# Performance work log

Hardware: AMD Instinct MI355X
Metric: run time of the kernel (lower is better)

The kernel has to match this reference:

```python
import jax, jax.numpy as jnp
import numpy as np

B, T, D = 4, 2048, 2048
NUM_EXPERTS = 64
TOP_K = 2


def setup_inputs() -> dict:
    key = jax.random.key(0)
    k_x, k_n, k_wg, k_wn = jax.random.split(key, 4)
    x = jax.random.normal(k_x, (B, T, D), dtype=jnp.float32)
    noise_eps = jax.random.normal(k_n, (B, T, NUM_EXPERTS), dtype=jnp.float32)
    # nn.Linear(D, E, bias=False): weight [E, D]; store transposed [D, E] for einsum
    scale = 1.0 / np.sqrt(D)
    w_gate = jax.random.uniform(k_wg, (D, NUM_EXPERTS), jnp.float32, -scale, scale)
    w_noise = jax.random.uniform(k_wn, (D, NUM_EXPERTS), jnp.float32, -scale, scale)
    return {"x": x, "noise_eps": noise_eps, "w_gate": w_gate, "w_noise": w_noise}


def reference(x, noise_eps, w_gate, w_noise):
    # gate + noisy logits: softplus(w_noise(x)) * randn_like (noise_eps passed in)
    logits = jnp.einsum("btd,de->bte", x, w_gate)
    noise = jax.nn.softplus(jnp.einsum("btd,de->bte", x, w_noise)) * noise_eps
    logits = logits + noise

    # top-k over experts
    top_k_logits, top_k_indices = jax.lax.top_k(logits, TOP_K)  # [B,T,K]

    # scatter(-inf fill) + softmax == softmax over top-k values scattered into E slots
    one_hot = jax.nn.one_hot(top_k_indices, NUM_EXPERTS, dtype=logits.dtype)  # [B,T,K,E]
    router_probs = jnp.einsum("btk,btke->bte", jax.nn.softmax(top_k_logits, axis=-1), one_hot)

    # per-expert mask: [num_tokens, K, E] -> permute(1,0,2) -> [K, num_tokens, E]
    exp_mask = one_hot.reshape(B * T, TOP_K, NUM_EXPERTS).transpose(1, 0, 2).astype(jnp.int32)
    return router_probs, top_k_indices, exp_mask
```

## Files before the change

kernel.cpp:

```cpp
#include <hip/hip_runtime.h>
#include <math.h>

#define DD    2048
#define EE    64
#define NTOK  8192
#define BM    32
#define NKS   32

#define PROB_OFF 0
#define IDX_OFF  524288
#define MASK_OFF 540672
#define MASK_K_STRIDE (NTOK * EE)

typedef __bf16 bf16x8 __attribute__((ext_vector_type(8)));
typedef float  f32x16 __attribute__((ext_vector_type(16)));

__device__ __forceinline__ unsigned f2bf_rne(float f) {
  unsigned u = __float_as_uint(f);
  return (u + 0x7fffu + ((u >> 16) & 1u)) >> 16;
}
__device__ __forceinline__ float bf2f(unsigned h) {
  return __uint_as_float(h << 16);
}

__global__ __launch_bounds__(256) void prep_w(
    const float* __restrict__ wg, const float* __restrict__ wn,
    unsigned char* __restrict__ wsb)
{
  const int t  = blockIdx.x * 256 + threadIdx.x;
  const int l  = t & 63;
  const int nt = (t >> 6) & 3;
  const int g  = t >> 8;
  const int colg = nt * 32 + (l & 31);
  const int kb   = g * 16 + 8 * (l >> 5);
  const float* wsrc = (colg < EE) ? (wg + colg) : (wn + (colg - EE));

  unsigned hv[8], lv[8];
#pragma unroll
  for (int i = 0; i < 8; ++i) {
    const float v = wsrc[(size_t)(kb + i) * EE];
    const unsigned h = f2bf_rne(v);
    hv[i] = h;
    lv[i] = f2bf_rne(v - bf2f(h));
  }
  uint4 hq, lq;
  hq.x = hv[0] | (hv[1] << 16); hq.y = hv[2] | (hv[3] << 16);
  hq.z = hv[4] | (hv[5] << 16); hq.w = hv[6] | (hv[7] << 16);
  lq.x = lv[0] | (lv[1] << 16); lq.y = lv[2] | (lv[3] << 16);
  lq.z = lv[4] | (lv[5] << 16); lq.w = lv[6] | (lv[7] << 16);

  const size_t base = ((size_t)(g * 4 + nt) * 2) * 1024 + (size_t)l * 16;
  *reinterpret_cast<uint4*>(wsb + base)        = hq;
  *reinterpret_cast<uint4*>(wsb + base + 1024) = lq;
}

struct KSet { float4 xa, xb; uint4 bh, bl; };

union BF8 { bf16x8 v; ushort u[8]; };

__device__ __forceinline__ void cvt_hilo(const float4& a, const float4& b,
                                         bf16x8& hi, bf16x8& lo) {
  const float f[8] = {a.x, a.y, a.z, a.w, b.x, b.y, b.z, b.w};
  BF8 H, L;
#pragma unroll
  for (int i = 0; i < 8; ++i) {
    const unsigned u = __float_as_uint(f[i]);
    H.u[i] = (ushort)(u >> 16);
    L.v[i] = (__bf16)(f[i] - __uint_as_float(u & 0xffff0000u));
  }
  hi = H.v; lo = L.v;
}

__global__ __launch_bounds__(1024, 4) void router_fused(
    const float* __restrict__ x,
    const float* __restrict__ noise_eps,
    const unsigned char* __restrict__ wsb,
    float* __restrict__ out)
{
  __shared__ float Lp[4][BM][128];

  const int tid  = threadIdx.x;
  const int wid  = tid >> 6;
  const int lane = tid & 63;
  const int nt   = wid & 3;
  const int kh   = wid >> 2;
  const int tok0 = blockIdx.x * BM;

  const float* xp = x + (size_t)(tok0 + (lane & 31)) * DD
                      + kh * 512 + 8 * (lane >> 5);
  const unsigned char* bp = wsb + ((size_t)(kh * 32) * 4 + nt) * 2048
                                + (size_t)lane * 16;

  auto LOAD = [&](int s) {
    KSet k;
    const float* p = xp + 16 * s;
    k.xa = *reinterpret_cast<const float4*>(p);
    k.xb = *reinterpret_cast<const float4*>(p + 4);
    const unsigned char* q = bp + (size_t)8192 * s;
    k.bh = *reinterpret_cast<const uint4*>(q);
    k.bl = *reinterpret_cast<const uint4*>(q + 1024);
    return k;
  };

  f32x16 acc = {0.f,0.f,0.f,0.f,0.f,0.f,0.f,0.f,
                0.f,0.f,0.f,0.f,0.f,0.f,0.f,0.f};

  auto COMPUTE = [&](const KSet& k) {
    bf16x8 ahi, alo;
    cvt_hilo(k.xa, k.xb, ahi, alo);
    const bf16x8 bhi = __builtin_bit_cast(bf16x8, k.bh);
    const bf16x8 blo = __builtin_bit_cast(bf16x8, k.bl);
    acc = __builtin_amdgcn_mfma_f32_32x32x16_bf16(ahi, bhi, acc, 0, 0, 0);
    acc = __builtin_amdgcn_mfma_f32_32x32x16_bf16(ahi, blo, acc, 0, 0, 0);
    acc = __builtin_amdgcn_mfma_f32_32x32x16_bf16(alo, bhi, acc, 0, 0, 0);
    acc = __builtin_amdgcn_mfma_f32_32x32x16_bf16(alo, blo, acc, 0, 0, 0);
  };

  KSet a = LOAD(0), b = LOAD(1);
#pragma unroll 1
  for (int s = 0; s < NKS - 2; s += 2) {
    KSet t0 = LOAD(s + 2);
    COMPUTE(a);
    a = t0;
    KSet t1 = LOAD(s + 3);
    COMPUTE(b);
    b = t1;
  }
  COMPUTE(a);
  COMPUTE(b);

  const int ccol  = nt * 32 + (lane & 31);
  const int crow0 = 4 * (lane >> 5);
#pragma unroll
  for (int q = 0; q < 16; ++q)
    Lp[kh][(q & 3) + 8 * (q >> 2) + crow0][ccol] = acc[q];
  __syncthreads();

#pragma unroll
  for (int it = 0; it < 2; ++it) {
    const int tl  = wid * 2 + it;
    const int tok = tok0 + tl;

    const float g    = Lp[0][tl][lane] + Lp[1][tl][lane]
                     + Lp[2][tl][lane] + Lp[3][tl][lane];
    const float nraw = Lp[0][tl][64 + lane] + Lp[1][tl][64 + lane]
                     + Lp[2][tl][64 + lane] + Lp[3][tl][64 + lane];
    const float ep   = noise_eps[(size_t)tok * EE + lane];

    const float sp = fmaxf(nraw, 0.0f) + log1pf(expf(-fabsf(nraw)));
    const float z  = fmaf(sp, ep, g);

    float v1 = z; int i1 = lane;
#pragma unroll
    for (int off = 32; off >= 1; off >>= 1) {
      const float ov = __shfl_xor(v1, off, 64);
      const int   oi = __shfl_xor(i1, off, 64);
      if (ov > v1 || (ov == v1 && oi < i1)) { v1 = ov; i1 = oi; }
    }
    float v2 = (lane == i1) ? -INFINITY : z; int i2 = lane;
#pragma unroll
    for (int off = 32; off >= 1; off >>= 1) {
      const float ov = __shfl_xor(v2, off, 64);
      const int   oi = __shfl_xor(i2, off, 64);
      if (ov > v2 || (ov == v2 && oi < i2)) { v2 = ov; i2 = oi; }
    }

    const float e2 = expf(v2 - v1);
    const float denom = 1.0f + e2;
    const float p1 = 1.0f / denom;
    const float p2 = e2 / denom;

    out[PROB_OFF + (size_t)tok * EE + lane] =
        (lane == i1) ? p1 : ((lane == i2) ? p2 : 0.0f);
    if (lane == 0) {
      out[IDX_OFF + tok * 2 + 0] = (float)i1;
      out[IDX_OFF + tok * 2 + 1] = (float)i2;
    }
    out[MASK_OFF + 0 * MASK_K_STRIDE + (size_t)tok * EE + lane] =
        (lane == i1) ? 1.0f : 0.0f;
    out[MASK_OFF + 1 * MASK_K_STRIDE + (size_t)tok * EE + lane] =
        (lane == i2) ? 1.0f : 0.0f;
  }
}

extern "C" void kernel_launch(void* const* d_in, const int* in_sizes, int n_in,
                              void* d_out, int out_size, void* d_ws, size_t ws_size,
                              hipStream_t stream) {
  const float* x   = (const float*)d_in[0];
  const float* eps = (const float*)d_in[1];
  const float* wg  = (const float*)d_in[2];
  const float* wn  = (const float*)d_in[3];
  unsigned char* wsb = (unsigned char*)d_ws;

  prep_w<<<dim3(128), dim3(256), 0, stream>>>(wg, wn, wsb);
  router_fused<<<dim3(NTOK / BM), dim3(1024), 0, stream>>>(x, eps, wsb,
                                                           (float*)d_out);
}
```

Baseline: 138.3 us.

## Reuse converted x fragments across four expert tiles per wave, drop lo*lo MFMA

Each block now uses 8 waves instead of 16. Each wave covers a 256-wide K slice for all 128 output columns, so one x load and its hi/lo bf16 conversion feed four accumulators. This removes the fourfold redundant x loading and conversion of the old per-column-tile wave split. The lo*lo MFMA term is dropped, trimming MFMA work by a quarter at a small accuracy cost. The pipeline becomes a fully unrolled 3-slot register prefetch, and partial sums are reduced through shared memory in two phases; this raises register pressure and may cut the latency hiding that came from running more waves.

```diff
diff --git a/kernel.cpp b/kernel.cpp
--- a/kernel.cpp
+++ b/kernel.cpp
@@ -5,7 +5,8 @@
 #define EE    64
 #define NTOK  8192
 #define BM    32
-#define NKS   32
+#define NKH   8
+#define NKS   16
 
 #define PROB_OFF 0
 #define IDX_OFF  524288
@@ -54,7 +55,10 @@
   *reinterpret_cast<uint4*>(wsb + base + 1024) = lq;
 }
 
-struct KSet { float4 xa, xb; uint4 bh, bl; };
+struct Slot {
+  float4 xa, xb;
+  uint4 bh0, bl0, bh1, bl1, bh2, bl2, bh3, bl3;
+};
 
 union BF8 { bf16x8 v; ushort u[8]; };
 
@@ -71,7 +75,57 @@
   hi = H.v; lo = L.v;
 }
 
-__global__ __launch_bounds__(1024, 4) void router_fused(
+__device__ __forceinline__ bf16x8 bc(const uint4& q) {
+  return __builtin_bit_cast(bf16x8, q);
+}
+
+__device__ __forceinline__ void load_slot(Slot& s, const float* xp,
+                                          const unsigned char* bp, int ks) {
+  const float* p = xp + 16 * ks;
+  s.xa = *reinterpret_cast<const float4*>(p);
+  s.xb = *reinterpret_cast<const float4*>(p + 4);
+  const unsigned char* q = bp + (size_t)8192 * ks;
+  s.bh0 = *reinterpret_cast<const uint4*>(q);
+  s.bl0 = *reinterpret_cast<const uint4*>(q + 1024);
+  s.bh1 = *reinterpret_cast<const uint4*>(q + 2048);
+  s.bl1 = *reinterpret_cast<const uint4*>(q + 3072);
+  s.bh2 = *reinterpret_cast<const uint4*>(q + 4096);
+  s.bl2 = *reinterpret_cast<const uint4*>(q + 5120);
+  s.bh3 = *reinterpret_cast<const uint4*>(q + 6144);
+  s.bl3 = *reinterpret_cast<const uint4*>(q + 7168);
+}
+
+__device__ __forceinline__ void compute_slot(const Slot& s,
+    f32x16& a0, f32x16& a1, f32x16& a2, f32x16& a3) {
+  bf16x8 ahi, alo;
+  cvt_hilo(s.xa, s.xb, ahi, alo);
+  {
+    const bf16x8 bh = bc(s.bh0), bl = bc(s.bl0);
+    a0 = __builtin_amdgcn_mfma_f32_32x32x16_bf16(ahi, bh, a0, 0, 0, 0);
+    a0 = __builtin_amdgcn_mfma_f32_32x32x16_bf16(ahi, bl, a0, 0, 0, 0);
+    a0 = __builtin_amdgcn_mfma_f32_32x32x16_bf16(alo, bh, a0, 0, 0, 0);
+  }
+  {
+    const bf16x8 bh = bc(s.bh1), bl = bc(s.bl1);
+    a1 = __builtin_amdgcn_mfma_f32_32x32x16_bf16(ahi, bh, a1, 0, 0, 0);
+    a1 = __builtin_amdgcn_mfma_f32_32x32x16_bf16(ahi, bl, a1, 0, 0, 0);
+    a1 = __builtin_amdgcn_mfma_f32_32x32x16_bf16(alo, bh, a1, 0, 0, 0);
+  }
+  {
+    const bf16x8 bh = bc(s.bh2), bl = bc(s.bl2);
+    a2 = __builtin_amdgcn_mfma_f32_32x32x16_bf16(ahi, bh, a2, 0, 0, 0);
+    a2 = __builtin_amdgcn_mfma_f32_32x32x16_bf16(ahi, bl, a2, 0, 0, 0);
+    a2 = __builtin_amdgcn_mfma_f32_32x32x16_bf16(alo, bh, a2, 0, 0, 0);
+  }
+  {
+    const bf16x8 bh = bc(s.bh3), bl = bc(s.bl3);
+    a3 = __builtin_amdgcn_mfma_f32_32x32x16_bf16(ahi, bh, a3, 0, 0, 0);
+    a3 = __builtin_amdgcn_mfma_f32_32x32x16_bf16(ahi, bl, a3, 0, 0, 0);
+    a3 = __builtin_amdgcn_mfma_f32_32x32x16_bf16(alo, bh, a3, 0, 0, 0);
+  }
+}
+
+__global__ __launch_bounds__(512, 2) void router_fused(
     const float* __restrict__ x,
     const float* __restrict__ noise_eps,
     const unsigned char* __restrict__ wsb,
@@ -82,63 +136,56 @@
   const int tid  = threadIdx.x;
   const int wid  = tid >> 6;
   const int lane = tid & 63;
-  const int nt   = wid & 3;
-  const int kh   = wid >> 2;
+  const int kh   = wid;
   const int tok0 = blockIdx.x * BM;
 
   const float* xp = x + (size_t)(tok0 + (lane & 31)) * DD
-                      + kh * 512 + 8 * (lane >> 5);
-  const unsigned char* bp = wsb + ((size_t)(kh * 32) * 4 + nt) * 2048
-                                + (size_t)lane * 16;
-
-  auto LOAD = [&](int s) {
-    KSet k;
-    const float* p = xp + 16 * s;
-    k.xa = *reinterpret_cast<const float4*>(p);
-    k.xb = *reinterpret_cast<const float4*>(p + 4);
-    const unsigned char* q = bp + (size_t)8192 * s;
-    k.bh = *reinterpret_cast<const uint4*>(q);
-    k.bl = *reinterpret_cast<const uint4*>(q + 1024);
-    return k;
-  };
-
-  f32x16 acc = {0.f,0.f,0.f,0.f,0.f,0.f,0.f,0.f,
-                0.f,0.f,0.f,0.f,0.f,0.f,0.f,0.f};
-
-  auto COMPUTE = [&](const KSet& k) {
-    bf16x8 ahi, alo;
-    cvt_hilo(k.xa, k.xb, ahi, alo);
-    const bf16x8 bhi = __builtin_bit_cast(bf16x8, k.bh);
-    const bf16x8 blo = __builtin_bit_cast(bf16x8, k.bl);
-    acc = __builtin_amdgcn_mfma_f32_32x32x16_bf16(ahi, bhi, acc, 0, 0, 0);
-    acc = __builtin_amdgcn_mfma_f32_32x32x16_bf16(ahi, blo, acc, 0, 0, 0);
-    acc = __builtin_amdgcn_mfma_f32_32x32x16_bf16(alo, bhi, acc, 0, 0, 0);
-    acc = __builtin_amdgcn_mfma_f32_32x32x16_bf16(alo, blo, acc, 0, 0, 0);
-  };
-
-  KSet a = LOAD(0), b = LOAD(1);
-#pragma unroll 1
-  for (int s = 0; s < NKS - 2; s += 2) {
-    KSet t0 = LOAD(s + 2);
-    COMPUTE(a);
-    a = t0;
-    KSet t1 = LOAD(s + 3);
-    COMPUTE(b);
-    b = t1;
-  }
-  COMPUTE(a);
-  COMPUTE(b);
-
-  const int ccol  = nt * 32 + (lane & 31);
+                      + kh * 256 + 8 * (lane >> 5);
+  const unsigned char* bp = wsb + (size_t)(kh * 16) * 8192 + (size_t)lane * 16;
+
+  f32x16 a0 = {0.f,0.f,0.f,0.f,0.f,0.f,0.f,0.f,0.f,0.f,0.f,0.f,0.f,0.f,0.f,0.f};
+  f32x16 a1 = a0, a2 = a0, a3 = a0;
+
+  Slot s0, s1, s2;
+  load_slot(s0, xp, bp, 0);
+  load_slot(s1, xp, bp, 1);
+  load_slot(s2, xp, bp, 2);
+
+#pragma unroll
+  for (int s = 0; s < NKS; ++s) {
+    Slot& cur = (s % 3 == 0) ? s0 : (s % 3 == 1) ? s1 : s2;
+    compute_slot(cur, a0, a1, a2, a3);
+    if (s + 3 < NKS) load_slot(cur, xp, bp, s + 3);
+  }
+
+  const int ccol0 = lane & 31;
   const int crow0 = 4 * (lane >> 5);
-#pragma unroll
-  for (int q = 0; q < 16; ++q)
-    Lp[kh][(q & 3) + 8 * (q >> 2) + crow0][ccol] = acc[q];
+  if (wid < 4) {
+#pragma unroll
+    for (int q = 0; q < 16; ++q) {
+      const int row = (q & 3) + 8 * (q >> 2) + crow0;
+      Lp[wid][row][ccol0]      = a0[q];
+      Lp[wid][row][32 + ccol0] = a1[q];
+      Lp[wid][row][64 + ccol0] = a2[q];
+      Lp[wid][row][96 + ccol0] = a3[q];
+    }
+  }
   __syncthreads();
-
-#pragma unroll
-  for (int it = 0; it < 2; ++it) {
-    const int tl  = wid * 2 + it;
+  if (wid >= 4) {
+#pragma unroll
+    for (int q = 0; q < 16; ++q) {
+      const int row = (q & 3) + 8 * (q >> 2) + crow0;
+      Lp[wid - 4][row][ccol0]      += a0[q];
+      Lp[wid - 4][row][32 + ccol0] += a1[q];
+      Lp[wid - 4][row][64 + ccol0] += a2[q];
+      Lp[wid - 4][row][96 + ccol0] += a3[q];
+    }
+  }
+  __syncthreads();
+
+#pragma unroll
+  for (int it = 0; it < 4; ++it) {
+    const int tl  = wid * 4 + it;
     const int tok = tok0 + tl;
 
     const float g    = Lp[0][tl][lane] + Lp[1][tl][lane]
@@ -193,6 +240,6 @@
   unsigned char* wsb = (unsigned char*)d_ws;
 
   prep_w<<<dim3(128), dim3(256), 0, stream>>>(wg, wn, wsb);
-  router_fused<<<dim3(NTOK / BM), dim3(1024), 0, stream>>>(x, eps, wsb,
-                                                           (float*)d_out);
-}
+  router_fused<<<dim3(NTOK / BM), dim3(512), 0, stream>>>(x, eps, wsb,
+                                                          (float*)d_out);
+}
```

New measurement: 127.6 us. 7.7% less time.

## Split-K router GEMM into separate kernel with workspace partials and epilogue kernel

Applied to the files above, without the earlier changes.

Replaces the single fused 1024-thread kernel with a split-K GEMM kernel (256 threads, grid over tokens x 4 K-slices) that writes partial logits to workspace, followed by a separate epilogue kernel doing the reduction, softplus, top-2, softmax and mask writes. Each wave now computes two N-tiles and drops the lo*lo MFMA term (3 MFMAs per tile instead of 4), and the explicit double-buffered prefetch is replaced by a fully unrolled loop. The aim is more blocks and better occupancy with less MFMA work. In exchange it adds partial-sum traffic through global memory, an extra kernel launch, and slightly lower precision from dropping the lo*lo term.

```diff
diff --git a/kernel.cpp b/kernel.cpp
--- a/kernel.cpp
+++ b/kernel.cpp
@@ -1,11 +1,12 @@
 #include <hip/hip_runtime.h>
 #include <math.h>
 
-#define DD    2048
-#define EE    64
-#define NTOK  8192
-#define BM    32
-#define NKS   32
+#define DD     2048
+#define EE     64
+#define NTOK   8192
+#define BM     32
+#define KSPLIT 4
+#define NKS    16
 
 #define PROB_OFF 0
 #define IDX_OFF  524288
@@ -54,8 +55,6 @@
   *reinterpret_cast<uint4*>(wsb + base + 1024) = lq;
 }
 
-struct KSet { float4 xa, xb; uint4 bh, bl; };
-
 union BF8 { bf16x8 v; ushort u[8]; };
 
 __device__ __forceinline__ void cvt_hilo(const float4& a, const float4& b,
@@ -71,116 +70,135 @@
   hi = H.v; lo = L.v;
 }
 
-__global__ __launch_bounds__(1024, 4) void router_fused(
+__device__ __forceinline__ bf16x8 bc(const uint4& q) {
+  return __builtin_bit_cast(bf16x8, q);
+}
+
+__global__ __launch_bounds__(256, 4) void router_gemm(
     const float* __restrict__ x,
+    const unsigned char* __restrict__ wsb,
+    float* __restrict__ part)
+{
+  __shared__ float Lp[BM][128];
+
+  const int tid  = threadIdx.x;
+  const int w    = tid >> 6;
+  const int lane = tid & 63;
+  const int nt2  = w & 1;
+  const int kq   = w >> 1;
+  const int tok0 = blockIdx.x * BM;
+  const int ks   = blockIdx.y;
+
+  const int kbase = ks * 512 + kq * 256;
+  const float* xp = x + (size_t)(tok0 + (lane & 31)) * DD
+                      + kbase + 8 * (lane >> 5);
+  const unsigned char* bp = wsb
+      + ((size_t)((kbase >> 4) * 4 + 2 * nt2)) * 2048 + (size_t)lane * 16;
+
+  f32x16 a0 = {0.f,0.f,0.f,0.f,0.f,0.f,0.f,0.f,0.f,0.f,0.f,0.f,0.f,0.f,0.f,0.f};
+  f32x16 a1 = a0;
+
+#pragma unroll
+  for (int s = 0; s < NKS; ++s) {
+    const float* p = xp + 16 * s;
+    const float4 xa = *reinterpret_cast<const float4*>(p);
+    const float4 xb = *reinterpret_cast<const float4*>(p + 4);
+    const unsigned char* q = bp + (size_t)8192 * s;
+    const uint4 bh0 = *reinterpret_cast<const uint4*>(q);
+    const uint4 bl0 = *reinterpret_cast<const uint4*>(q + 1024);
+    const uint4 bh1 = *reinterpret_cast<const uint4*>(q + 2048);
+    const uint4 bl1 = *reinterpret_cast<const uint4*>(q + 3072);
+
+    bf16x8 ahi, alo;
+    cvt_hilo(xa, xb, ahi, alo);
+    a0 = __builtin_amdgcn_mfma_f32_32x32x16_bf16(ahi, bc(bh0), a0, 0, 0, 0);
+    a0 = __builtin_amdgcn_mfma_f32_32x32x16_bf16(ahi, bc(bl0), a0, 0, 0, 0);
+    a0 = __builtin_amdgcn_mfma_f32_32x32x16_bf16(alo, bc(bh0), a0, 0, 0, 0);
+    a1 = __builtin_amdgcn_mfma_f32_32x32x16_bf16(ahi, bc(bh1), a1, 0, 0, 0);
+    a1 = __builtin_amdgcn_mfma_f32_32x32x16_bf16(ahi, bc(bl1), a1, 0, 0, 0);
+    a1 = __builtin_amdgcn_mfma_f32_32x32x16_bf16(alo, bc(bh1), a1, 0, 0, 0);
+  }
+
+  const int ccol  = 64 * nt2 + (lane & 31);
+  const int crow0 = 4 * (lane >> 5);
+  if (kq == 0) {
+#pragma unroll
+    for (int q = 0; q < 16; ++q) {
+      const int row = (q & 3) + 8 * (q >> 2) + crow0;
+      Lp[row][ccol]      = a0[q];
+      Lp[row][ccol + 32] = a1[q];
+    }
+  }
+  __syncthreads();
+  if (kq == 1) {
+#pragma unroll
+    for (int q = 0; q < 16; ++q) {
+      const int row = (q & 3) + 8 * (q >> 2) + crow0;
+      Lp[row][ccol]      += a0[q];
+      Lp[row][ccol + 32] += a1[q];
+    }
+  }
+  __syncthreads();
+
+#pragma unroll
+  for (int rr = 0; rr < 8; ++rr) {
+    const int r = 8 * w + rr;
+    const float2 v = *reinterpret_cast<const float2*>(&Lp[r][2 * lane]);
+    *reinterpret_cast<float2*>(
+        part + ((size_t)(tok0 + r) * KSPLIT + ks) * 128 + 2 * lane) = v;
+  }
+}
+
+__global__ __launch_bounds__(256) void router_epilogue(
+    const float* __restrict__ part,
     const float* __restrict__ noise_eps,
-    const unsigned char* __restrict__ wsb,
     float* __restrict__ out)
 {
-  __shared__ float Lp[4][BM][128];
-
-  const int tid  = threadIdx.x;
-  const int wid  = tid >> 6;
-  const int lane = tid & 63;
-  const int nt   = wid & 3;
-  const int kh   = wid >> 2;
-  const int tok0 = blockIdx.x * BM;
-
-  const float* xp = x + (size_t)(tok0 + (lane & 31)) * DD
-                      + kh * 512 + 8 * (lane >> 5);
-  const unsigned char* bp = wsb + ((size_t)(kh * 32) * 4 + nt) * 2048
-                                + (size_t)lane * 16;
-
-  auto LOAD = [&](int s) {
-    KSet k;
-    const float* p = xp + 16 * s;
-    k.xa = *reinterpret_cast<const float4*>(p);
-    k.xb = *reinterpret_cast<const float4*>(p + 4);
-    const unsigned char* q = bp + (size_t)8192 * s;
-    k.bh = *reinterpret_cast<const uint4*>(q);
-    k.bl = *reinterpret_cast<const uint4*>(q + 1024);
-    return k;
-  };
-
-  f32x16 acc = {0.f,0.f,0.f,0.f,0.f,0.f,0.f,0.f,
-                0.f,0.f,0.f,0.f,0.f,0.f,0.f,0.f};
-
-  auto COMPUTE = [&](const KSet& k) {
-    bf16x8 ahi, alo;
-    cvt_hilo(k.xa, k.xb, ahi, alo);
-    const bf16x8 bhi = __builtin_bit_cast(bf16x8, k.bh);
-    const bf16x8 blo = __builtin_bit_cast(bf16x8, k.bl);
-    acc = __builtin_amdgcn_mfma_f32_32x32x16_bf16(ahi, bhi, acc, 0, 0, 0);
-    acc = __builtin_amdgcn_mfma_f32_32x32x16_bf16(ahi, blo, acc, 0, 0, 0);
-    acc = __builtin_amdgcn_mfma_f32_32x32x16_bf16(alo, bhi, acc, 0, 0, 0);
-    acc = __builtin_amdgcn_mfma_f32_32x32x16_bf16(alo, blo, acc, 0, 0, 0);
-  };
-
-  KSet a = LOAD(0), b = LOAD(1);
-#pragma unroll 1
-  for (int s = 0; s < NKS - 2; s += 2) {
-    KSet t0 = LOAD(s + 2);
-    COMPUTE(a);
-    a = t0;
-    KSet t1 = LOAD(s + 3);
-    COMPUTE(b);
-    b = t1;
-  }
-  COMPUTE(a);
-  COMPUTE(b);
-
-  const int ccol  = nt * 32 + (lane & 31);
-  const int crow0 = 4 * (lane >> 5);
-#pragma unroll
-  for (int q = 0; q < 16; ++q)
-    Lp[kh][(q & 3) + 8 * (q >> 2) + crow0][ccol] = acc[q];
-  __syncthreads();
-
-#pragma unroll
-  for (int it = 0; it < 2; ++it) {
-    const int tl  = wid * 2 + it;
-    const int tok = tok0 + tl;
-
-    const float g    = Lp[0][tl][lane] + Lp[1][tl][lane]
-                     + Lp[2][tl][lane] + Lp[3][tl][lane];
-    const float nraw = Lp[0][tl][64 + lane] + Lp[1][tl][64 + lane]
-                     + Lp[2][tl][64 + lane] + Lp[3][tl][64 + lane];
-    const float ep   = noise_eps[(size_t)tok * EE + lane];
-
-    const float sp = fmaxf(nraw, 0.0f) + log1pf(expf(-fabsf(nraw)));
-    const float z  = fmaf(sp, ep, g);
-
-    float v1 = z; int i1 = lane;
-#pragma unroll
-    for (int off = 32; off >= 1; off >>= 1) {
-      const float ov = __shfl_xor(v1, off, 64);
-      const int   oi = __shfl_xor(i1, off, 64);
-      if (ov > v1 || (ov == v1 && oi < i1)) { v1 = ov; i1 = oi; }
-    }
-    float v2 = (lane == i1) ? -INFINITY : z; int i2 = lane;
-#pragma unroll
-    for (int off = 32; off >= 1; off >>= 1) {
-      const float ov = __shfl_xor(v2, off, 64);
-      const int   oi = __shfl_xor(i2, off, 64);
-      if (ov > v2 || (ov == v2 && oi < i2)) { v2 = ov; i2 = oi; }
-    }
-
-    const float e2 = expf(v2 - v1);
-    const float denom = 1.0f + e2;
-    const float p1 = 1.0f / denom;
-    const float p2 = e2 / denom;
-
-    out[PROB_OFF + (size_t)tok * EE + lane] =
-        (lane == i1) ? p1 : ((lane == i2) ? p2 : 0.0f);
-    if (lane == 0) {
-      out[IDX_OFF + tok * 2 + 0] = (float)i1;
-      out[IDX_OFF + tok * 2 + 1] = (float)i2;
-    }
-    out[MASK_OFF + 0 * MASK_K_STRIDE + (size_t)tok * EE + lane] =
-        (lane == i1) ? 1.0f : 0.0f;
-    out[MASK_OFF + 1 * MASK_K_STRIDE + (size_t)tok * EE + lane] =
-        (lane == i2) ? 1.0f : 0.0f;
-  }
+  const int t    = blockIdx.x * 4 + (threadIdx.x >> 6);
+  const int lane = threadIdx.x & 63;
+
+  const float* p = part + (size_t)t * KSPLIT * 128;
+  float g = 0.0f, nraw = 0.0f;
+#pragma unroll
+  for (int s = 0; s < KSPLIT; ++s) {
+    g    += p[s * 128 + lane];
+    nraw += p[s * 128 + EE + lane];
+  }
+  const float ep = noise_eps[(size_t)t * EE + lane];
+
+  const float sp = fmaxf(nraw, 0.0f) + log1pf(expf(-fabsf(nraw)));
+  const float z  = fmaf(sp, ep, g);
+
+  float v1 = z; int i1 = lane;
+#pragma unroll
+  for (int off = 32; off >= 1; off >>= 1) {
+    const float ov = __shfl_xor(v1, off, 64);
+    const int   oi = __shfl_xor(i1, off, 64);
+    if (ov > v1 || (ov == v1 && oi < i1)) { v1 = ov; i1 = oi; }
+  }
+  float v2 = (lane == i1) ? -INFINITY : z; int i2 = lane;
+#pragma unroll
+  for (int off = 32; off >= 1; off >>= 1) {
+    const float ov = __shfl_xor(v2, off, 64);
+    const int   oi = __shfl_xor(i2, off, 64);
+    if (ov > v2 || (ov == v2 && oi < i2)) { v2 = ov; i2 = oi; }
+  }
+
+  const float e2 = expf(v2 - v1);
+  const float denom = 1.0f + e2;
+  const float p1 = 1.0f / denom;
+  const float p2 = e2 / denom;
+
+  out[PROB_OFF + (size_t)t * EE + lane] =
+      (lane == i1) ? p1 : ((lane == i2) ? p2 : 0.0f);
+
+  if (lane == 0) {
+    out[IDX_OFF + t * 2 + 0] = (float)i1;
+    out[IDX_OFF + t * 2 + 1] = (float)i2;
+  }
+
+  out[MASK_OFF + 0 * MASK_K_STRIDE + (size_t)t * EE + lane] = (lane == i1) ? 1.0f : 0.0f;
+  out[MASK_OFF + 1 * MASK_K_STRIDE + (size_t)t * EE + lane] = (lane == i2) ? 1.0f : 0.0f;
 }
 
 extern "C" void kernel_launch(void* const* d_in, const int* in_sizes, int n_in,
@@ -190,9 +208,12 @@
   const float* eps = (const float*)d_in[1];
   const float* wg  = (const float*)d_in[2];
   const float* wn  = (const float*)d_in[3];
+
   unsigned char* wsb = (unsigned char*)d_ws;
+  float* part = (float*)(wsb + (1 << 20));
 
   prep_w<<<dim3(128), dim3(256), 0, stream>>>(wg, wn, wsb);
-  router_fused<<<dim3(NTOK / BM), dim3(1024), 0, stream>>>(x, eps, wsb,
-                                                           (float*)d_out);
-}
+  router_gemm<<<dim3(NTOK / BM, KSPLIT), dim3(256), 0, stream>>>(x, wsb, part);
+  router_epilogue<<<dim3(NTOK / 4), dim3(256), 0, stream>>>(part, eps,
+                                                            (float*)d_out);
+}
```

Measured after the change: 137.1 us. About the same (-0.9%).
